# Performance work log

Hardware: AMD Instinct MI355X
Metric: run time of the kernel (lower is better)

Reference implementation:

```python
import jax, jax.numpy as jnp
import numpy as np

N = 50000
E = 800000
IN_C = 128
HID_C = 64
OUT_C = 64
HEADS = 4
NEG_SLOPE = 0.2


def setup_inputs() -> dict:
    key = jax.random.key(0)
    ks = jax.random.split(key, 12)
    x = jax.random.normal(ks[0], (N, IN_C), dtype=jnp.float32)
    edge_index = jax.random.randint(ks[1], (2, E), 0, N, dtype=jnp.int32)
    s = 0.1
    # layer 1 params (GATConv: shared lin for src/dst, att vectors per head, bias over H*C)
    W1 = jax.random.normal(ks[2], (IN_C, HEADS * HID_C), dtype=jnp.float32) * s
    att_src1 = jax.random.normal(ks[3], (HEADS, HID_C), dtype=jnp.float32) * s
    att_dst1 = jax.random.normal(ks[4], (HEADS, HID_C), dtype=jnp.float32) * s
    b1 = jnp.zeros((HEADS * HID_C,), dtype=jnp.float32)
    # layer 2 params
    W2 = jax.random.normal(ks[5], (HEADS * HID_C, HEADS * OUT_C), dtype=jnp.float32) * s
    att_src2 = jax.random.normal(ks[6], (HEADS, OUT_C), dtype=jnp.float32) * s
    att_dst2 = jax.random.normal(ks[7], (HEADS, OUT_C), dtype=jnp.float32) * s
    b2 = jnp.zeros((HEADS * OUT_C,), dtype=jnp.float32)
    return {"x": x, "edge_index": edge_index,
            "W1": W1, "att_src1": att_src1, "att_dst1": att_dst1, "b1": b1,
            "W2": W2, "att_src2": att_src2, "att_dst2": att_dst2, "b2": b2}


def _segment_softmax(e, dst, n):
    # e: [E, H], softmax over edges sharing the same dst node, per head
    m = jax.ops.segment_max(e, dst, num_segments=n)        # [N, H]
    ex = jnp.exp(e - m[dst])
    z = jax.ops.segment_sum(ex, dst, num_segments=n)       # [N, H]
    return ex / (z[dst] + 1e-16)


def _gat_layer(x, src, dst, W, att_src, att_dst, bias, heads, out_c):
    n = x.shape[0]
    h = (x @ W).reshape(n, heads, out_c)                   # [N, H, C]
    a_s = jnp.einsum('nhc,hc->nh', h, att_src)             # [N, H]
    a_d = jnp.einsum('nhc,hc->nh', h, att_dst)
    e = jax.nn.leaky_relu(a_s[src] + a_d[dst], NEG_SLOPE)  # [E, H]
    alpha = _segment_softmax(e, dst, n)                    # [E, H]
    msg = alpha[:, :, None] * h[src]                       # [E, H, C]
    out = jax.ops.segment_sum(msg, dst, num_segments=n)    # [N, H, C]
    return out.reshape(n, heads * out_c) + bias


def reference(x, edge_index, W1, att_src1, att_dst1, b1, W2, att_src2, att_dst2, b2):
    # PyG GATConv adds self-loops by default
    loops = jnp.arange(N, dtype=edge_index.dtype)
    src = jnp.concatenate([edge_index[0], loops])
    dst = jnp.concatenate([edge_index[1], loops])
    h = jax.nn.elu(_gat_layer(x, src, dst, W1, att_src1, att_dst1, b1, HEADS, HID_C))
    out = jax.nn.elu(_gat_layer(h, src, dst, W2, att_src2, att_dst2, b2, HEADS, OUT_C))
    return out  # [N, HEADS*OUT_C]
```

## Files before the change

### kernel.cpp

```cpp
#include <hip/hip_runtime.h>
#include <hip/hip_fp16.h>
#include <math.h>


#define LEAKY_SLOPE 0.2f

typedef __attribute__((ext_vector_type(8))) short short8v;
typedef __attribute__((ext_vector_type(4))) float float4v;


__global__ void hist_kernel(const int* __restrict__ ei, int* __restrict__ cnt,
                            int E, int Etot) {
    int e = blockIdx.x * blockDim.x + threadIdx.x;
    if (e >= Etot) return;
    int dst = (e < E) ? ei[E + e] : (e - E);
    atomicAdd(&cnt[dst], 1);
}

__global__ __launch_bounds__(1024) void scan_block(const int* __restrict__ cnt,
                                                   int* __restrict__ row_start,
                                                   int* __restrict__ partials,
                                                   int n) {
    __shared__ int wsum[16];
    int tid = threadIdx.x, lane = tid & 63, wid = tid >> 6;
    int gi = blockIdx.x * 1024 + tid;
    int v = (gi < n) ? cnt[gi] : 0;
    int x = v;
#pragma unroll
    for (int off = 1; off < 64; off <<= 1) {
        int y = __shfl_up(x, off, 64);
        if (lane >= off) x += y;
    }
    if (lane == 63) wsum[wid] = x;
    __syncthreads();
    if (wid == 0 && lane < 16) {
        int w = wsum[lane];
#pragma unroll
        for (int off = 1; off < 16; off <<= 1) {
            int y = __shfl_up(w, off, 16);
            if (lane >= off) w += y;
        }
        wsum[lane] = w;
    }
    __syncthreads();
    int excl = x - v + ((wid > 0) ? wsum[wid - 1] : 0);
    if (gi < n) row_start[gi] = excl;
    if (tid == 1023) partials[blockIdx.x] = wsum[15];
}

__global__ void scan_partials(int* __restrict__ partials, int nb) {
    int lane = threadIdx.x;
    int v = (lane < nb) ? partials[lane] : 0;
    int x = v;
#pragma unroll
    for (int off = 1; off < 64; off <<= 1) {
        int y = __shfl_up(x, off, 64);
        if (lane >= off) x += y;
    }
    if (lane < nb) partials[lane] = x - v;
    if (lane == nb - 1) partials[nb] = x;
}

__global__ __launch_bounds__(1024) void scan_add(int* __restrict__ row_start,
                                                 const int* __restrict__ partials,
                                                 int n, int nb) {
    int gi = blockIdx.x * 1024 + threadIdx.x;
    if (gi < n) row_start[gi] += partials[blockIdx.x];
    if (gi == 0) row_start[n] = partials[nb];
}

__global__ void scatter_kernel(const int* __restrict__ ei,
                               const int* __restrict__ row_start,
                               int* __restrict__ fill,
                               int* __restrict__ edge_src, int E, int Etot) {
    int e = blockIdx.x * blockDim.x + threadIdx.x;
    if (e >= Etot) return;
    int src, dst;
    if (e < E) { src = ei[e]; dst = ei[E + e]; }
    else       { src = e - E; dst = e - E; }
    int pos = row_start[dst] + atomicAdd(&fill[dst], 1);
    edge_src[pos] = src;
}

__global__ void fill_rec(const int* __restrict__ edge_src,
                         const __half* __restrict__ a_s_h,
                         uint4* __restrict__ rec, int Etot) {
    int i = blockIdx.x * blockDim.x + threadIdx.x;
    if (i >= Etot) return;
    int s = edge_src[i];
    uint2 as8 = *(const uint2*)&a_s_h[(size_t)s * 4];
    uint4 r = {(unsigned)s, as8.x, as8.y, 0u};
    rec[i] = r;
}


__device__ __forceinline__ short bf16_rne(float f) {
    unsigned u = __float_as_uint(f);
    return (short)((u + 0x7FFFu + ((u >> 16) & 1u)) >> 16);
}

__device__ __forceinline__ void split_bf16(float f, short& hi, short& lo) {
    unsigned u = __float_as_uint(f);
    hi = (short)(u >> 16);
    float fhi = __uint_as_float(u & 0xFFFF0000u);
    float flo = f - fhi;
    lo = (short)(__float_as_uint(flo) >> 16);
}

template <int K, bool ABF16>
__global__ __launch_bounds__(256) void gemm_mfma(
    const void* __restrict__ Ap, const float* __restrict__ B,
    __half* __restrict__ Ch, const float* __restrict__ att_src,
    const float* __restrict__ att_dst, __half* __restrict__ a_s_out,
    float* __restrict__ a_d_out, int M) {
    __shared__ short As_hi[128][40];
    __shared__ short Bs_hi[128][40];
    __shared__ short Bs_lo[128][40];

    const int col0 = (blockIdx.x & 1) * 128;
    const int row0 = (blockIdx.x >> 1) * 128;
    const int tid = threadIdx.x;
    const int lane = tid & 63;
    const int wave = tid >> 6;
    const int wr = wave >> 1, wc = wave & 1;
    const int quad = lane >> 4, lc = lane & 15;

    float4v acc[4][4] = {};

    const int bn = tid & 127;
    const int bkh = (tid >> 7) * 16;

    for (int k0 = 0; k0 < K; k0 += 32) {
        if constexpr (ABF16) {
            const short* Abf = (const short*)Ap;
#pragma unroll
            for (int i = 0; i < 2; i++) {
                int slot = tid + i * 256;
                int r = slot >> 2;
                int ko = (slot & 3) * 8;
                short8v v = {};
                int gr = row0 + r;
                if (gr < M) v = *(const short8v*)&Abf[(size_t)gr * K + k0 + ko];
                short4 lo4 = {v[0], v[1], v[2], v[3]};
                short4 hi4 = {v[4], v[5], v[6], v[7]};
                *(short4*)&As_hi[r][ko] = lo4;
                *(short4*)&As_hi[r][ko + 4] = hi4;
            }
        } else {
            const float* A = (const float*)Ap;
#pragma unroll
            for (int i = 0; i < 4; i++) {
                int slot = tid + i * 256;
                int r = slot >> 3;
                int kq = (slot & 7) * 4;
                float4 v = {0.f, 0.f, 0.f, 0.f};
                int gr = row0 + r;
                if (gr < M) v = *(const float4*)&A[(size_t)gr * K + k0 + kq];
                short4 h4;
                h4.x = bf16_rne(v.x); h4.y = bf16_rne(v.y);
                h4.z = bf16_rne(v.z); h4.w = bf16_rne(v.w);
                *(short4*)&As_hi[r][kq] = h4;
            }
        }
        {
            float f[16];
#pragma unroll
            for (int j = 0; j < 16; j++)
                f[j] = B[(size_t)(k0 + bkh + j) * 256 + col0 + bn];
            short h8[16], l8[16];
#pragma unroll
            for (int j = 0; j < 16; j++) split_bf16(f[j], h8[j], l8[j]);
#pragma unroll
            for (int j = 0; j < 4; j++) {
                *(short4*)&Bs_hi[bn][bkh + j * 4] = *(short4*)&h8[j * 4];
                *(short4*)&Bs_lo[bn][bkh + j * 4] = *(short4*)&l8[j * 4];
            }
        }
        __syncthreads();

        short8v a_hi[4], b_hi[4], b_lo[4];
#pragma unroll
        for (int mt = 0; mt < 4; mt++) {
            int r = wr * 64 + mt * 16 + lc;
            a_hi[mt] = *(const short8v*)&As_hi[r][quad * 8];
        }
#pragma unroll
        for (int nt = 0; nt < 4; nt++) {
            int n = wc * 64 + nt * 16 + lc;
            b_hi[nt] = *(const short8v*)&Bs_hi[n][quad * 8];
            b_lo[nt] = *(const short8v*)&Bs_lo[n][quad * 8];
        }
#pragma unroll
        for (int mt = 0; mt < 4; mt++)
#pragma unroll
            for (int nt = 0; nt < 4; nt++) {
                acc[mt][nt] = __builtin_amdgcn_mfma_f32_16x16x32_bf16(
                    a_hi[mt], b_hi[nt], acc[mt][nt], 0, 0, 0);
                acc[mt][nt] = __builtin_amdgcn_mfma_f32_16x16x32_bf16(
                    a_hi[mt], b_lo[nt], acc[mt][nt], 0, 0, 0);
            }
        __syncthreads();
    }

    const int head = (col0 >> 6) + wc;
    float as_c[4], ad_c[4];
#pragma unroll
    for (int nt = 0; nt < 4; nt++) {
        as_c[nt] = att_src[head * 64 + nt * 16 + lc];
        ad_c[nt] = att_dst[head * 64 + nt * 16 + lc];
    }

#pragma unroll
    for (int mt = 0; mt < 4; mt++) {
#pragma unroll
        for (int r = 0; r < 4; r++) {
            int gr = row0 + wr * 64 + mt * 16 + quad * 4 + r;
            float ps = 0.f, pd = 0.f;
#pragma unroll
            for (int nt = 0; nt < 4; nt++) {
                float c = acc[mt][nt][r];
                ps = fmaf(c, as_c[nt], ps);
                pd = fmaf(c, ad_c[nt], pd);
                if (gr < M)
                    Ch[(size_t)gr * 256 + col0 + wc * 64 + nt * 16 + lc] =
                        __float2half(c);
            }
#pragma unroll
            for (int off = 1; off < 16; off <<= 1) {
                ps += __shfl_xor(ps, off, 64);
                pd += __shfl_xor(pd, off, 64);
            }
            if (lc == 0 && gr < M) {
                a_s_out[gr * 4 + head] = __float2half(ps);
                a_d_out[gr * 4 + head] = pd;
            }
        }
    }
}


template <bool OUT_BF16>
__global__ __launch_bounds__(256) void gat_aggregate(
    const __half* __restrict__ hh, const uint4* __restrict__ rec,
    const float* __restrict__ a_d, const int* __restrict__ row_start,
    const float* __restrict__ bias, void* __restrict__ outp, int n) {
    int wid = (blockIdx.x * blockDim.x + threadIdx.x) >> 6;
    int lane = threadIdx.x & 63;
    int half = lane >> 5, l32 = lane & 31;
    int node = wid * 2 + half;
    bool valid = (node < n);
    int nd = valid ? node : 0;
    int head = l32 >> 3;

    float ad = a_d[nd * 4 + head];
    int beg = row_start[nd];
    int end = valid ? row_start[nd + 1] : beg;

    float l = 0.f;
    float acc[8] = {};

    int em1 = (end > beg) ? (end - 1) : beg;
    uint4 r0 = rec[beg];
    uint4 r1 = rec[min(beg + 1, em1)];
    uint4 r2 = rec[min(beg + 2, em1)];

#define GATH(rr) (*(const uint4*)&hh[(size_t)(rr).x * 256 + l32 * 8])
#define PROC(rr, vv)                                                      \
    {                                                                     \
        unsigned u = (head & 2) ? (rr).z : (rr).y;                        \
        unsigned short us = (head & 1) ? (unsigned short)(u >> 16)        \
                                       : (unsigned short)(u & 0xFFFFu);   \
        float as = __half2float(*(const __half*)&us);                     \
        float e = as + ad;                                                \
        e = (e > 0.f) ? e : LEAKY_SLOPE * e;                              \
        float w = __expf(e);                                              \
        l += w;                                                           \
        const __half2* hp = (const __half2*)&(vv);                        \
        _Pragma("unroll") for (int j = 0; j < 4; j++) {                   \
            float2 f = __half22float2(hp[j]);                             \
            acc[2 * j] = fmaf(w, f.x, acc[2 * j]);                        \
            acc[2 * j + 1] = fmaf(w, f.y, acc[2 * j + 1]);                \
        }                                                                 \
    }

    uint4 h0 = GATH(r0);
    uint4 h1 = GATH(r1);
    uint4 h2;

    int s = beg;
    while (s < end) {
        h2 = GATH(r2);
        PROC(r0, h0);
        r0 = rec[min(s + 3, em1)];
        if (++s >= end) break;
        h0 = GATH(r0);
        PROC(r1, h1);
        r1 = rec[min(s + 3, em1)];
        if (++s >= end) break;
        h1 = GATH(r1);
        PROC(r2, h2);
        r2 = rec[min(s + 3, em1)];
        ++s;
    }
#undef GATH
#undef PROC

    if (valid) {
        float r = 1.f / l;
        float4 b0 = *(const float4*)&bias[l32 * 8];
        float4 b1 = *(const float4*)&bias[l32 * 8 + 4];
        float o[8];
        o[0] = fmaf(acc[0], r, b0.x); o[1] = fmaf(acc[1], r, b0.y);
        o[2] = fmaf(acc[2], r, b0.z); o[3] = fmaf(acc[3], r, b0.w);
        o[4] = fmaf(acc[4], r, b1.x); o[5] = fmaf(acc[5], r, b1.y);
        o[6] = fmaf(acc[6], r, b1.z); o[7] = fmaf(acc[7], r, b1.w);
#pragma unroll
        for (int j = 0; j < 8; j++)
            o[j] = (o[j] > 0.f) ? o[j] : __expf(o[j]) - 1.f;
        if constexpr (OUT_BF16) {
            short ob[8];
#pragma unroll
            for (int j = 0; j < 8; j++) ob[j] = bf16_rne(o[j]);
            short* outb = (short*)outp;
            *(short4*)&outb[(size_t)node * 256 + l32 * 8] = *(short4*)&ob[0];
            *(short4*)&outb[(size_t)node * 256 + l32 * 8 + 4] = *(short4*)&ob[4];
        } else {
            float* outf = (float*)outp;
            *(float4*)&outf[(size_t)node * 256 + l32 * 8] = *(float4*)&o[0];
            *(float4*)&outf[(size_t)node * 256 + l32 * 8 + 4] = *(float4*)&o[4];
        }
    }
}


extern "C" void kernel_launch(void* const* d_in, const int* in_sizes, int n_in,
                              void* d_out, int out_size, void* d_ws, size_t ws_size,
                              hipStream_t stream) {
    const float* x   = (const float*)d_in[0];
    const int*   ei  = (const int*)d_in[1];
    const float* W1  = (const float*)d_in[2];
    const float* as1 = (const float*)d_in[3];
    const float* ad1 = (const float*)d_in[4];
    const float* b1  = (const float*)d_in[5];
    const float* W2  = (const float*)d_in[6];
    const float* as2 = (const float*)d_in[7];
    const float* ad2 = (const float*)d_in[8];
    const float* b2  = (const float*)d_in[9];
    float* out = (float*)d_out;

    const int N = in_sizes[0] / 128;
    const int E = in_sizes[1] / 2;
    const int Etot = E + N;
    const int NB = (N + 1023) / 1024;

    __half* h_half = (__half*)d_ws;
    short*  x1_bf  = (short*)(h_half + (size_t)N * 256);
    uint4*  rec    = (uint4*)(x1_bf + (size_t)N * 256);
    __half* a_s_h  = (__half*)(rec + Etot);
    float*  a_d    = (float*)(a_s_h + (size_t)N * 4);
    int*    cnt    = (int*)(a_d + (size_t)N * 4);
    int*    fill   = cnt + N;
    int*    row_st = fill + N;
    int*    edge_src = row_st + (N + 1);
    int*    partials = edge_src + Etot;

    hipMemsetAsync(cnt, 0, sizeof(int) * 2 * (size_t)N, stream);
    int eblocks = (Etot + 255) / 256;
    hist_kernel<<<eblocks, 256, 0, stream>>>(ei, cnt, E, Etot);
    scan_block<<<NB, 1024, 0, stream>>>(cnt, row_st, partials, N);
    scan_partials<<<1, 64, 0, stream>>>(partials, NB);
    scan_add<<<NB, 1024, 0, stream>>>(row_st, partials, N, NB);
    scatter_kernel<<<eblocks, 256, 0, stream>>>(ei, row_st, fill, edge_src, E, Etot);

    dim3 ggrid(2 * ((N + 127) / 128));
    int ablocks = (N + 7) / 8;

    gemm_mfma<128, false><<<ggrid, 256, 0, stream>>>(x, W1, h_half, as1, ad1,
                                                     a_s_h, a_d, N);
    fill_rec<<<eblocks, 256, 0, stream>>>(edge_src, a_s_h, rec, Etot);
    gat_aggregate<true><<<ablocks, 256, 0, stream>>>(h_half, rec, a_d, row_st,
                                                     b1, x1_bf, N);
    gemm_mfma<256, true><<<ggrid, 256, 0, stream>>>(x1_bf, W2, h_half, as2, ad2,
                                                    a_s_h, a_d, N);
    fill_rec<<<eblocks, 256, 0, stream>>>(edge_src, a_s_h, rec, Etot);
    gat_aggregate<false><<<ablocks, 256, 0, stream>>>(h_half, rec, a_d, row_st,
                                                      b2, out, N);
}
```

Before: 396.2 us.

## Pre-convert x and transposed split-bf16 weights; add nontemporal loads/stores

Adds pre-pass kernels that convert x to bf16 and transpose W1/W2 into split hi/lo bf16 arrays, so the GEMM tiles load contiguous short8 vectors instead of converting fp32 and reading B column-strided in every block. The record loads in aggregation and the output and record stores become nontemporal. This removes redundant per-block weight conversion but adds three extra launches and an extra pass over x.

Result: slower. 419.4 us (+5.9%).

```diff
diff --git a/kernel.cpp b/kernel.cpp
--- a/kernel.cpp
+++ b/kernel.cpp
@@ -6,7 +6,57 @@
 #define LEAKY_SLOPE 0.2f
 
 typedef __attribute__((ext_vector_type(8))) short short8v;
+typedef __attribute__((ext_vector_type(4))) short short4n;
 typedef __attribute__((ext_vector_type(4))) float float4v;
+typedef __attribute__((ext_vector_type(4))) unsigned int uint4v;
+
+__device__ __forceinline__ short bf16_rne(float f) {
+    unsigned u = __float_as_uint(f);
+    return (short)((u + 0x7FFFu + ((u >> 16) & 1u)) >> 16);
+}
+
+__device__ __forceinline__ void split_bf16(float f, short& hi, short& lo) {
+    unsigned u = __float_as_uint(f);
+    hi = (short)(u >> 16);
+    float fhi = __uint_as_float(u & 0xFFFF0000u);
+    float flo = f - fhi;
+    lo = (short)(__float_as_uint(flo) >> 16);
+}
+
+
+__global__ void conv_x(const float* __restrict__ x, short* __restrict__ xb,
+                       int n4) {
+    int i = blockIdx.x * blockDim.x + threadIdx.x;
+    if (i >= n4) return;
+    float4 v = ((const float4*)x)[i];
+    short4 s;
+    s.x = bf16_rne(v.x); s.y = bf16_rne(v.y);
+    s.z = bf16_rne(v.z); s.w = bf16_rne(v.w);
+    ((short4*)xb)[i] = s;
+}
+
+__global__ __launch_bounds__(256) void conv_W(const float* __restrict__ W,
+                                              short* __restrict__ Wt_hi,
+                                              short* __restrict__ Wt_lo, int K) {
+    __shared__ float tile[32][33];
+    int tx = threadIdx.x & 31, ty = threadIdx.x >> 5;
+    int bx = blockIdx.x, by = blockIdx.y;
+#pragma unroll
+    for (int i = 0; i < 4; i++) {
+        int k = by * 32 + ty + i * 8;
+        tile[ty + i * 8][tx] = W[(size_t)k * 256 + bx * 32 + tx];
+    }
+    __syncthreads();
+#pragma unroll
+    for (int i = 0; i < 4; i++) {
+        int n = bx * 32 + ty + i * 8;
+        float f = tile[tx][ty + i * 8];
+        short hi, lo;
+        split_bf16(f, hi, lo);
+        Wt_hi[(size_t)n * K + by * 32 + tx] = hi;
+        Wt_lo[(size_t)n * K + by * 32 + tx] = lo;
+    }
+}
 
 
 __global__ void hist_kernel(const int* __restrict__ ei, int* __restrict__ cnt,
@@ -84,38 +134,25 @@
 
 __global__ void fill_rec(const int* __restrict__ edge_src,
                          const __half* __restrict__ a_s_h,
-                         uint4* __restrict__ rec, int Etot) {
+                         uint4v* __restrict__ rec, int Etot) {
     int i = blockIdx.x * blockDim.x + threadIdx.x;
     if (i >= Etot) return;
     int s = edge_src[i];
     uint2 as8 = *(const uint2*)&a_s_h[(size_t)s * 4];
-    uint4 r = {(unsigned)s, as8.x, as8.y, 0u};
-    rec[i] = r;
-}
-
-
-__device__ __forceinline__ short bf16_rne(float f) {
-    unsigned u = __float_as_uint(f);
-    return (short)((u + 0x7FFFu + ((u >> 16) & 1u)) >> 16);
-}
-
-__device__ __forceinline__ void split_bf16(float f, short& hi, short& lo) {
-    unsigned u = __float_as_uint(f);
-    hi = (short)(u >> 16);
-    float fhi = __uint_as_float(u & 0xFFFF0000u);
-    float flo = f - fhi;
-    lo = (short)(__float_as_uint(flo) >> 16);
-}
-
-template <int K, bool ABF16>
+    uint4v r = {(unsigned)s, as8.x, as8.y, 0u};
+    __builtin_nontemporal_store(r, &rec[i]);
+}
+
+
+template <int K>
 __global__ __launch_bounds__(256) void gemm_mfma(
-    const void* __restrict__ Ap, const float* __restrict__ B,
-    __half* __restrict__ Ch, const float* __restrict__ att_src,
-    const float* __restrict__ att_dst, __half* __restrict__ a_s_out,
-    float* __restrict__ a_d_out, int M) {
-    __shared__ short As_hi[128][40];
-    __shared__ short Bs_hi[128][40];
-    __shared__ short Bs_lo[128][40];
+    const short* __restrict__ A, const short* __restrict__ Bth,
+    const short* __restrict__ Btl, __half* __restrict__ Ch,
+    const float* __restrict__ att_src, const float* __restrict__ att_dst,
+    __half* __restrict__ a_s_out, float* __restrict__ a_d_out, int M) {
+    __shared__ short As[128][40];
+    __shared__ short Bh[128][40];
+    __shared__ short Bl[128][40];
 
     const int col0 = (blockIdx.x & 1) * 128;
     const int row0 = (blockIdx.x >> 1) * 128;
@@ -127,77 +164,49 @@
 
     float4v acc[4][4] = {};
 
-    const int bn = tid & 127;
-    const int bkh = (tid >> 7) * 16;
-
     for (int k0 = 0; k0 < K; k0 += 32) {
-        if constexpr (ABF16) {
-            const short* Abf = (const short*)Ap;
-#pragma unroll
-            for (int i = 0; i < 2; i++) {
-                int slot = tid + i * 256;
-                int r = slot >> 2;
-                int ko = (slot & 3) * 8;
-                short8v v = {};
-                int gr = row0 + r;
-                if (gr < M) v = *(const short8v*)&Abf[(size_t)gr * K + k0 + ko];
-                short4 lo4 = {v[0], v[1], v[2], v[3]};
-                short4 hi4 = {v[4], v[5], v[6], v[7]};
-                *(short4*)&As_hi[r][ko] = lo4;
-                *(short4*)&As_hi[r][ko + 4] = hi4;
-            }
-        } else {
-            const float* A = (const float*)Ap;
-#pragma unroll
-            for (int i = 0; i < 4; i++) {
-                int slot = tid + i * 256;
-                int r = slot >> 3;
-                int kq = (slot & 7) * 4;
-                float4 v = {0.f, 0.f, 0.f, 0.f};
-                int gr = row0 + r;
-                if (gr < M) v = *(const float4*)&A[(size_t)gr * K + k0 + kq];
-                short4 h4;
-                h4.x = bf16_rne(v.x); h4.y = bf16_rne(v.y);
-                h4.z = bf16_rne(v.z); h4.w = bf16_rne(v.w);
-                *(short4*)&As_hi[r][kq] = h4;
-            }
-        }
-        {
-            float f[16];
-#pragma unroll
-            for (int j = 0; j < 16; j++)
-                f[j] = B[(size_t)(k0 + bkh + j) * 256 + col0 + bn];
-            short h8[16], l8[16];
-#pragma unroll
-            for (int j = 0; j < 16; j++) split_bf16(f[j], h8[j], l8[j]);
-#pragma unroll
-            for (int j = 0; j < 4; j++) {
-                *(short4*)&Bs_hi[bn][bkh + j * 4] = *(short4*)&h8[j * 4];
-                *(short4*)&Bs_lo[bn][bkh + j * 4] = *(short4*)&l8[j * 4];
-            }
+#pragma unroll
+        for (int i = 0; i < 2; i++) {
+            int slot = tid + i * 256;
+            int r = slot >> 2;
+            int c8 = (slot & 3) * 8;
+            short8v v = {};
+            int gr = row0 + r;
+            if (gr < M) v = *(const short8v*)&A[(size_t)gr * K + k0 + c8];
+            *(short8v*)&As[r][c8] = v;
+        }
+#pragma unroll
+        for (int i = 0; i < 2; i++) {
+            int slot = tid + i * 256;
+            int n = slot >> 2;
+            int c8 = (slot & 3) * 8;
+            *(short8v*)&Bh[n][c8] =
+                *(const short8v*)&Bth[(size_t)(col0 + n) * K + k0 + c8];
+            *(short8v*)&Bl[n][c8] =
+                *(const short8v*)&Btl[(size_t)(col0 + n) * K + k0 + c8];
         }
         __syncthreads();
 
-        short8v a_hi[4], b_hi[4], b_lo[4];
+        short8v a_f[4], b_hi[4], b_lo[4];
 #pragma unroll
         for (int mt = 0; mt < 4; mt++) {
             int r = wr * 64 + mt * 16 + lc;
-            a_hi[mt] = *(const short8v*)&As_hi[r][quad * 8];
+            a_f[mt] = *(const short8v*)&As[r][quad * 8];
         }
 #pragma unroll
         for (int nt = 0; nt < 4; nt++) {
             int n = wc * 64 + nt * 16 + lc;
-            b_hi[nt] = *(const short8v*)&Bs_hi[n][quad * 8];
-            b_lo[nt] = *(const short8v*)&Bs_lo[n][quad * 8];
+            b_hi[nt] = *(const short8v*)&Bh[n][quad * 8];
+            b_lo[nt] = *(const short8v*)&Bl[n][quad * 8];
         }
 #pragma unroll
         for (int mt = 0; mt < 4; mt++)
 #pragma unroll
             for (int nt = 0; nt < 4; nt++) {
                 acc[mt][nt] = __builtin_amdgcn_mfma_f32_16x16x32_bf16(
-                    a_hi[mt], b_hi[nt], acc[mt][nt], 0, 0, 0);
+                    a_f[mt], b_hi[nt], acc[mt][nt], 0, 0, 0);
                 acc[mt][nt] = __builtin_amdgcn_mfma_f32_16x16x32_bf16(
-                    a_hi[mt], b_lo[nt], acc[mt][nt], 0, 0, 0);
+                    a_f[mt], b_lo[nt], acc[mt][nt], 0, 0, 0);
             }
         __syncthreads();
     }
@@ -241,7 +250,7 @@
 
 template <bool OUT_BF16>
 __global__ __launch_bounds__(256) void gat_aggregate(
-    const __half* __restrict__ hh, const uint4* __restrict__ rec,
+    const __half* __restrict__ hh, const uint4v* __restrict__ rec,
     const float* __restrict__ a_d, const int* __restrict__ row_start,
     const float* __restrict__ bias, void* __restrict__ outp, int n) {
     int wid = (blockIdx.x * blockDim.x + threadIdx.x) >> 6;
@@ -260,11 +269,11 @@
     float acc[8] = {};
 
     int em1 = (end > beg) ? (end - 1) : beg;
-    uint4 r0 = rec[beg];
-    uint4 r1 = rec[min(beg + 1, em1)];
-    uint4 r2 = rec[min(beg + 2, em1)];
-
-#define GATH(rr) (*(const uint4*)&hh[(size_t)(rr).x * 256 + l32 * 8])
+    uint4v r0 = __builtin_nontemporal_load(&rec[beg]);
+    uint4v r1 = __builtin_nontemporal_load(&rec[min(beg + 1, em1)]);
+    uint4v r2 = __builtin_nontemporal_load(&rec[min(beg + 2, em1)]);
+
+#define GATH(rr) (*(const uint4v*)&hh[(size_t)(rr).x * 256 + l32 * 8])
 #define PROC(rr, vv)                                                      \
     {                                                                     \
         unsigned u = (head & 2) ? (rr).z : (rr).y;                        \
@@ -283,23 +292,23 @@
         }                                                                 \
     }
 
-    uint4 h0 = GATH(r0);
-    uint4 h1 = GATH(r1);
-    uint4 h2;
+    uint4v h0 = GATH(r0);
+    uint4v h1 = GATH(r1);
+    uint4v h2;
 
     int s = beg;
     while (s < end) {
         h2 = GATH(r2);
         PROC(r0, h0);
-        r0 = rec[min(s + 3, em1)];
+        r0 = __builtin_nontemporal_load(&rec[min(s + 3, em1)]);
         if (++s >= end) break;
         h0 = GATH(r0);
         PROC(r1, h1);
-        r1 = rec[min(s + 3, em1)];
+        r1 = __builtin_nontemporal_load(&rec[min(s + 3, em1)]);
         if (++s >= end) break;
         h1 = GATH(r1);
         PROC(r2, h2);
-        r2 = rec[min(s + 3, em1)];
+        r2 = __builtin_nontemporal_load(&rec[min(s + 3, em1)]);
         ++s;
     }
 #undef GATH
@@ -318,16 +327,24 @@
         for (int j = 0; j < 8; j++)
             o[j] = (o[j] > 0.f) ? o[j] : __expf(o[j]) - 1.f;
         if constexpr (OUT_BF16) {
-            short ob[8];
-#pragma unroll
-            for (int j = 0; j < 8; j++) ob[j] = bf16_rne(o[j]);
+            short4n ob0, ob1;
+            ob0.x = bf16_rne(o[0]); ob0.y = bf16_rne(o[1]);
+            ob0.z = bf16_rne(o[2]); ob0.w = bf16_rne(o[3]);
+            ob1.x = bf16_rne(o[4]); ob1.y = bf16_rne(o[5]);
+            ob1.z = bf16_rne(o[6]); ob1.w = bf16_rne(o[7]);
             short* outb = (short*)outp;
-            *(short4*)&outb[(size_t)node * 256 + l32 * 8] = *(short4*)&ob[0];
-            *(short4*)&outb[(size_t)node * 256 + l32 * 8 + 4] = *(short4*)&ob[4];
+            __builtin_nontemporal_store(ob0,
+                (short4n*)&outb[(size_t)node * 256 + l32 * 8]);
+            __builtin_nontemporal_store(ob1,
+                (short4n*)&outb[(size_t)node * 256 + l32 * 8 + 4]);
         } else {
+            float4v of0 = {o[0], o[1], o[2], o[3]};
+            float4v of1 = {o[4], o[5], o[6], o[7]};
             float* outf = (float*)outp;
-            *(float4*)&outf[(size_t)node * 256 + l32 * 8] = *(float4*)&o[0];
-            *(float4*)&outf[(size_t)node * 256 + l32 * 8 + 4] = *(float4*)&o[4];
+            __builtin_nontemporal_store(of0,
+                (float4v*)&outf[(size_t)node * 256 + l32 * 8]);
+            __builtin_nontemporal_store(of1,
+                (float4v*)&outf[(size_t)node * 256 + l32 * 8 + 4]);
         }
     }
 }
@@ -355,14 +372,23 @@
 
     __half* h_half = (__half*)d_ws;
     short*  x1_bf  = (short*)(h_half + (size_t)N * 256);
-    uint4*  rec    = (uint4*)(x1_bf + (size_t)N * 256);
-    __half* a_s_h  = (__half*)(rec + Etot);
+    uint4v* rec    = (uint4v*)(x1_bf + (size_t)N * 256);
+    short*  x_bf   = (short*)(rec + Etot);
+    short*  W1t_hi = x_bf + (size_t)N * 128;
+    short*  W1t_lo = W1t_hi + 256 * 128;
+    short*  W2t_hi = W1t_lo + 256 * 128;
+    short*  W2t_lo = W2t_hi + 256 * 256;
+    __half* a_s_h  = (__half*)(W2t_lo + 256 * 256);
     float*  a_d    = (float*)(a_s_h + (size_t)N * 4);
     int*    cnt    = (int*)(a_d + (size_t)N * 4);
     int*    fill   = cnt + N;
     int*    row_st = fill + N;
     int*    edge_src = row_st + (N + 1);
     int*    partials = edge_src + Etot;
+
+    conv_x<<<(N * 128 / 4 + 255) / 256, 256, 0, stream>>>(x, x_bf, N * 128 / 4);
+    conv_W<<<dim3(8, 128 / 32), 256, 0, stream>>>(W1, W1t_hi, W1t_lo, 128);
+    conv_W<<<dim3(8, 256 / 32), 256, 0, stream>>>(W2, W2t_hi, W2t_lo, 256);
 
     hipMemsetAsync(cnt, 0, sizeof(int) * 2 * (size_t)N, stream);
     int eblocks = (Etot + 255) / 256;
@@ -375,13 +401,13 @@
     dim3 ggrid(2 * ((N + 127) / 128));
     int ablocks = (N + 7) / 8;
 
-    gemm_mfma<128, false><<<ggrid, 256, 0, stream>>>(x, W1, h_half, as1, ad1,
-                                                     a_s_h, a_d, N);
+    gemm_mfma<128><<<ggrid, 256, 0, stream>>>(x_bf, W1t_hi, W1t_lo, h_half,
+                                              as1, ad1, a_s_h, a_d, N);
     fill_rec<<<eblocks, 256, 0, stream>>>(edge_src, a_s_h, rec, Etot);
     gat_aggregate<true><<<ablocks, 256, 0, stream>>>(h_half, rec, a_d, row_st,
                                                      b1, x1_bf, N);
-    gemm_mfma<256, true><<<ggrid, 256, 0, stream>>>(x1_bf, W2, h_half, as2, ad2,
-                                                    a_s_h, a_d, N);
+    gemm_mfma<256><<<ggrid, 256, 0, stream>>>(x1_bf, W2t_hi, W2t_lo, h_half,
+                                              as2, ad2, a_s_h, a_d, N);
     fill_rec<<<eblocks, 256, 0, stream>>>(edge_src, a_s_h, rec, Etot);
     gat_aggregate<false><<<ablocks, 256, 0, stream>>>(h_half, rec, a_d, row_st,
                                                       b2, out, N);
```
